# Optimization experiments

Hardware: AMD Instinct MI355X
Metric: run time of the kernel (lower is better)

Reference implementation:

```python
import jax, jax.numpy as jnp
import numpy as np

EPS = 1e-5  # torch LayerNorm default


def setup_inputs() -> dict:
    key = jax.random.key(0)
    k_x, k_wc, k_w = jax.random.split(key, 3)
    B, S, D = 16, 512, 2048
    x = jax.random.normal(k_x, (B, S, D), dtype=jnp.float32)
    # LayerNorm params
    gamma = jnp.ones((D,), dtype=jnp.float32)
    beta = jnp.zeros((D,), dtype=jnp.float32)
    # router (spatial_cls) Linear(d_ffn, 4)
    Wc = jax.random.normal(k_wc, (D, 4), dtype=jnp.float32) * 0.02
    bc = jnp.zeros((4,), dtype=jnp.float32)
    # 4 pointwise Conv1d experts: kernel size 1 over seq channels -> [4, S, S]
    W = jax.random.normal(k_w, (4, S, S), dtype=jnp.float32) * (1.0 / np.sqrt(S))
    # biases initialised to constants -1.0, -0.5, 0.5, 1.0 per expert
    b = jnp.stack([
        jnp.full((S,), -1.0, dtype=jnp.float32),
        jnp.full((S,), -0.5, dtype=jnp.float32),
        jnp.full((S,), 0.5, dtype=jnp.float32),
        jnp.full((S,), 1.0, dtype=jnp.float32),
    ])
    return {"x": x, "gamma": gamma, "beta": beta, "Wc": Wc, "bc": bc, "W": W, "b": b}


def reference(x, gamma, beta, Wc, bc, W, b):
    # LayerNorm over last dim
    mu = jnp.mean(x, axis=-1, keepdims=True)
    var = jnp.mean(jnp.square(x - mu), axis=-1, keepdims=True)
    y = (x - mu) * jax.lax.rsqrt(var + EPS) * gamma + beta
    # router: computed as in the original, but (faithfully to the source bug)
    # NOT used for dispatch -- dispatch uses the batch index n, clamped to 3.
    cls = jax.nn.softmax(y[:, 0] @ Wc + bc, axis=-1)
    _cls_idx = jnp.argmax(cls, axis=-1)  # computed, unused (original bug)
    eidx = jnp.minimum(jnp.arange(x.shape[0]), 3)  # sample n -> expert min(n,3)
    # pointwise Conv1d == seq-mixing matmul: out[b,s,d] = sum_t W_e[s,t] y[b,t,d] + b_e[s]
    out = jnp.einsum('bst,btd->bsd', W[eidx], y) + b[eidx][:, :, None]
    return jax.nn.gelu(out, approximate=False) + x
```

## Files before the change

### kernel.cpp

```cpp
#include <hip/hip_runtime.h>
#include <hip/hip_bf16.h>
#include <math.h>

#define NB 16
#define NS 512
#define ND 2048

typedef __attribute__((ext_vector_type(4))) float  f32x4v;
typedef __attribute__((ext_vector_type(8))) short  short8v;
typedef __attribute__((ext_vector_type(4))) float  accv;

__device__ __forceinline__ unsigned short f2bf(float f) {
  union { float f; unsigned u; } v; v.f = f;
  unsigned r = v.u + 0x7FFFu + ((v.u >> 16) & 1u);
  return (unsigned short)(r >> 16);
}

__device__ __forceinline__ int swz(int r, int kq) { return r * 4 + (kq ^ ((r >> 1) & 3)); }

#define GLL16(gp, lp) __builtin_amdgcn_global_load_lds(                        \
    (const __attribute__((address_space(1))) void*)(gp),                       \
    (__attribute__((address_space(3))) void*)(lp), 16, 0, 0)

__global__ __launch_bounds__(256) void k_meanvar(const float* __restrict__ x,
                                                 float* __restrict__ mv) {
  int row  = blockIdx.x * 4 + (threadIdx.x >> 6);
  int lane = threadIdx.x & 63;
  const float* xr = x + (size_t)row * ND;
  float s = 0.f, ss = 0.f;
#pragma unroll
  for (int q = 0; q < 8; ++q) {
    f32x4v v = *reinterpret_cast<const f32x4v*>(xr + q * 256 + lane * 4);
#pragma unroll
    for (int j = 0; j < 4; ++j) { s += v[j]; ss += v[j] * v[j]; }
  }
#pragma unroll
  for (int off = 1; off < 64; off <<= 1) {
    s  += __shfl_xor(s, off);
    ss += __shfl_xor(ss, off);
  }
  if (lane == 0) {
    float mean = s * (1.0f / ND);
    float var  = ss * (1.0f / ND) - mean * mean;
    mv[2 * row]     = mean;
    mv[2 * row + 1] = rsqrtf(var + 1e-5f);
  }
}

__global__ __launch_bounds__(256) void k_wcvt(const float* __restrict__ W,
                                              unsigned short* __restrict__ Aimg) {
  int ks = blockIdx.x, mp = blockIdx.y, e = blockIdx.z;
  size_t img = ((size_t)(e * 4 + mp) * 16 + ks) * 4096;
  int tid = threadIdx.x;
#pragma unroll
  for (int u = 0; u < 2; ++u) {
    int p = u * 256 + tid;
    int r = p >> 2, cc = p & 3;
    int kq = cc ^ ((r >> 1) & 3);
    const float* src = W + ((size_t)e * NS + mp * 128 + r) * NS + ks * 32 + kq * 8;
    f32x4v v0 = *reinterpret_cast<const f32x4v*>(src);
    f32x4v v1 = *reinterpret_cast<const f32x4v*>(src + 4);
    short8v o;
#pragma unroll
    for (int j = 0; j < 4; ++j) { o[j] = (short)f2bf(v0[j]); o[4 + j] = (short)f2bf(v1[j]); }
    *reinterpret_cast<short8v*>(Aimg + img + (size_t)p * 8) = o;
  }
}

__global__ __launch_bounds__(256) void k_normT(const float* __restrict__ x,
                                               const float* __restrict__ mv,
                                               const float* __restrict__ gamma,
                                               const float* __restrict__ beta,
                                               unsigned short* __restrict__ Bimg) {
  int d0 = blockIdx.x * 64, t0 = blockIdx.y * 64, bb = blockIdx.z;
  __shared__ unsigned int lds[64 * 32];
  int tid = threadIdx.x;
  {
    int tl = tid >> 2;
    int c  = tid & 3;
    int trow = bb * NS + t0 + tl;
    float mean = mv[2 * trow], rstd = mv[2 * trow + 1];
    const float* xr = x + (size_t)trow * ND + d0;
    int k = tl & 31;
#pragma unroll
    for (int q = 0; q < 4; ++q) {
      int dl = c * 16 + q * 4;
      f32x4v v = *reinterpret_cast<const f32x4v*>(xr + dl);
      f32x4v g = *reinterpret_cast<const f32x4v*>(gamma + d0 + dl);
      f32x4v b = *reinterpret_cast<const f32x4v*>(beta + d0 + dl);
      unsigned short h[4];
#pragma unroll
      for (int j = 0; j < 4; ++j) h[j] = f2bf((v[j] - mean) * rstd * g[j] + b[j]);
      lds[tl * 32 + (((dl >> 1)    ) ^ k)] = (unsigned)h[0] | ((unsigned)h[1] << 16);
      lds[tl * 32 + (((dl >> 1) + 1) ^ k)] = (unsigned)h[2] | ((unsigned)h[3] << 16);
    }
  }
  __syncthreads();
  {
    int dl = tid >> 2;
    int tc = (tid & 3) * 16;
    short8v o0, o1;
#pragma unroll
    for (int i = 0; i < 16; ++i) {
      int t = tc + i;
      unsigned w = lds[t * 32 + ((dl >> 1) ^ (t & 31))];
      unsigned short val = (dl & 1) ? (unsigned short)(w >> 16)
                                    : (unsigned short)(w & 0xffffu);
      if (i < 8) o0[i] = (short)val; else o1[i - 8] = (short)val;
    }
    int d  = d0 + dl;
    int np = d >> 7, r = d & 127;
    int tb  = t0 + tc;
    int ks  = tb >> 5;
    int kq0 = (tb >> 3) & 3;
    size_t img = ((size_t)(bb * 16 + np) * 16 + ks) * 4096;
    *reinterpret_cast<short8v*>(Bimg + img + (size_t)swz(r, kq0)     * 8) = o0;
    *reinterpret_cast<short8v*>(Bimg + img + (size_t)swz(r, kq0 + 1) * 8) = o1;
  }
}

__global__ __launch_bounds__(256) void k_gemm(const unsigned short* __restrict__ Aimg,
                                              const unsigned short* __restrict__ Bimg,
                                              const float* __restrict__ bias,
                                              const float* __restrict__ x,
                                              float* __restrict__ out) {
  int np = blockIdx.x, mp = blockIdx.y, bb = blockIdx.z;
  int e = bb < 3 ? bb : 3;
  const char* Abase = (const char*)(Aimg + ((size_t)(e  * 4 + mp) * 16) * 4096);
  const char* Bbase = (const char*)(Bimg + ((size_t)(bb * 16 + np) * 16) * 4096);
  __shared__ unsigned short Al[4096];
  __shared__ unsigned short Bl[4096];
  int tid = threadIdx.x;
  int lane = tid & 63, wid = tid >> 6;
  int wr = wid >> 1, wc = wid & 1;
  int lr = lane & 15, kq = lane >> 4;

  int aoff[4], boff[4];
#pragma unroll
  for (int mi = 0; mi < 4; ++mi) { int rr = wr * 64 + mi * 16 + lr; aoff[mi] = swz(rr, kq) * 8; }
#pragma unroll
  for (int ni = 0; ni < 4; ++ni) { int rr = wc * 64 + ni * 16 + lr; boff[ni] = swz(rr, kq) * 8; }

  accv acc[4][4] = {};

  for (int ks = 0; ks < 16; ++ks) {
#pragma unroll
    for (int i = 0; i < 2; ++i) {
      GLL16(Abase + ks * 8192 + i * 4096 + tid * 16, (char*)Al + i * 4096 + wid * 1024);
      GLL16(Bbase + ks * 8192 + i * 4096 + tid * 16, (char*)Bl + i * 4096 + wid * 1024);
    }
    __syncthreads();
    short8v a[4], b[4];
#pragma unroll
    for (int mi = 0; mi < 4; ++mi) a[mi] = *reinterpret_cast<const short8v*>(&Al[aoff[mi]]);
#pragma unroll
    for (int ni = 0; ni < 4; ++ni) b[ni] = *reinterpret_cast<const short8v*>(&Bl[boff[ni]]);
#pragma unroll
    for (int mi = 0; mi < 4; ++mi)
#pragma unroll
      for (int ni = 0; ni < 4; ++ni)
        acc[mi][ni] = __builtin_amdgcn_mfma_f32_16x16x32_bf16(a[mi], b[ni], acc[mi][ni], 0, 0, 0);
    __syncthreads();
  }

  const float* bp = bias + (size_t)e * NS;
  int m0 = mp * 128, n0 = np * 128;
#pragma unroll
  for (int mi = 0; mi < 4; ++mi) {
#pragma unroll
    for (int ni = 0; ni < 4; ++ni) {
#pragma unroll
      for (int r = 0; r < 4; ++r) {
        int s = m0 + wr * 64 + mi * 16 + ((lane >> 4) * 4) + r;
        int d = n0 + wc * 64 + ni * 16 + (lane & 15);
        float v = acc[mi][ni][r] + bp[s];
        float u = 1.5957691216f * (v + 0.044715f * v * v * v);
        float g = v / (1.0f + __expf(-u));
        size_t idx = ((size_t)bb * NS + s) * ND + d;
        out[idx] = g + x[idx];
      }
    }
  }
}

extern "C" void kernel_launch(void* const* d_in, const int* in_sizes, int n_in,
                              void* d_out, int out_size, void* d_ws, size_t ws_size,
                              hipStream_t stream) {
  const float* x     = (const float*)d_in[0];
  const float* gamma = (const float*)d_in[1];
  const float* beta  = (const float*)d_in[2];
  const float* W     = (const float*)d_in[5];
  const float* bias  = (const float*)d_in[6];
  float* out = (float*)d_out;

  unsigned short* Aimg = (unsigned short*)d_ws;
  float*          mv   = (float*)((char*)d_ws + (2ull << 20));
  unsigned short* Bimg = (unsigned short*)((char*)d_ws + (2ull << 20) + (64ull << 10));

  k_meanvar<<<NB * NS / 4, 256, 0, stream>>>(x, mv);
  k_wcvt<<<dim3(16, 4, 4), 256, 0, stream>>>(W, Aimg);
  k_normT<<<dim3(ND / 64, NS / 64, NB), 256, 0, stream>>>(x, mv, gamma, beta, Bimg);
  k_gemm<<<dim3(ND / 128, NS / 128, NB), 256, 0, stream>>>(Aimg, Bimg, bias, x, out);
}
```

Baseline: 177.0 us.

## Fuse LayerNorm stats into transpose kernel and double-buffer GEMM LDS loads

Merges the mean/variance pass and the normalize-transpose pass into one kernel that keeps each row in registers, so x is read once instead of twice. The normalized bf16 output is now written as a plain transposed [d][t] array. The GEMM swizzles that array on load through global_load_lds and double-buffers its LDS tiles, which removes one barrier per k-step. The cost is heavy register use in the LN kernel and more shared memory in the GEMM.

```diff
diff --git a/kernel.cpp b/kernel.cpp
--- a/kernel.cpp
+++ b/kernel.cpp
@@ -22,31 +22,6 @@
     (const __attribute__((address_space(1))) void*)(gp),                       \
     (__attribute__((address_space(3))) void*)(lp), 16, 0, 0)
 
-__global__ __launch_bounds__(256) void k_meanvar(const float* __restrict__ x,
-                                                 float* __restrict__ mv) {
-  int row  = blockIdx.x * 4 + (threadIdx.x >> 6);
-  int lane = threadIdx.x & 63;
-  const float* xr = x + (size_t)row * ND;
-  float s = 0.f, ss = 0.f;
-#pragma unroll
-  for (int q = 0; q < 8; ++q) {
-    f32x4v v = *reinterpret_cast<const f32x4v*>(xr + q * 256 + lane * 4);
-#pragma unroll
-    for (int j = 0; j < 4; ++j) { s += v[j]; ss += v[j] * v[j]; }
-  }
-#pragma unroll
-  for (int off = 1; off < 64; off <<= 1) {
-    s  += __shfl_xor(s, off);
-    ss += __shfl_xor(ss, off);
-  }
-  if (lane == 0) {
-    float mean = s * (1.0f / ND);
-    float var  = ss * (1.0f / ND) - mean * mean;
-    mv[2 * row]     = mean;
-    mv[2 * row + 1] = rsqrtf(var + 1e-5f);
-  }
-}
-
 __global__ __launch_bounds__(256) void k_wcvt(const float* __restrict__ W,
                                               unsigned short* __restrict__ Aimg) {
   int ks = blockIdx.x, mp = blockIdx.y, e = blockIdx.z;
@@ -67,69 +42,72 @@
   }
 }
 
-__global__ __launch_bounds__(256) void k_normT(const float* __restrict__ x,
-                                               const float* __restrict__ mv,
-                                               const float* __restrict__ gamma,
-                                               const float* __restrict__ beta,
-                                               unsigned short* __restrict__ Bimg) {
-  int d0 = blockIdx.x * 64, t0 = blockIdx.y * 64, bb = blockIdx.z;
-  __shared__ unsigned int lds[64 * 32];
+__global__ __launch_bounds__(512) void k_ln(const float* __restrict__ x,
+                                            const float* __restrict__ gamma,
+                                            const float* __restrict__ beta,
+                                            unsigned short* __restrict__ yT) {
+  int t0 = blockIdx.x * 32;
+  int bb = blockIdx.y;
   int tid = threadIdx.x;
-  {
-    int tl = tid >> 2;
-    int c  = tid & 3;
-    int trow = bb * NS + t0 + tl;
-    float mean = mv[2 * trow], rstd = mv[2 * trow + 1];
-    const float* xr = x + (size_t)trow * ND + d0;
-    int k = tl & 31;
+  int tA  = tid >> 4;
+  int dqA = (tid & 15) * 4;
+  const float* xr = x + ((size_t)bb * NS + t0 + tA) * ND + dqA;
+  f32x4v xv[32];
 #pragma unroll
-    for (int q = 0; q < 4; ++q) {
-      int dl = c * 16 + q * 4;
-      f32x4v v = *reinterpret_cast<const f32x4v*>(xr + dl);
-      f32x4v g = *reinterpret_cast<const f32x4v*>(gamma + d0 + dl);
-      f32x4v b = *reinterpret_cast<const f32x4v*>(beta + d0 + dl);
-      unsigned short h[4];
+  for (int k = 0; k < 32; ++k) xv[k] = *reinterpret_cast<const f32x4v*>(xr + k * 64);
+  float s = 0.f, ss = 0.f;
 #pragma unroll
-      for (int j = 0; j < 4; ++j) h[j] = f2bf((v[j] - mean) * rstd * g[j] + b[j]);
-      lds[tl * 32 + (((dl >> 1)    ) ^ k)] = (unsigned)h[0] | ((unsigned)h[1] << 16);
-      lds[tl * 32 + (((dl >> 1) + 1) ^ k)] = (unsigned)h[2] | ((unsigned)h[3] << 16);
+  for (int k = 0; k < 32; ++k)
+#pragma unroll
+    for (int j = 0; j < 4; ++j) { float f = xv[k][j]; s += f; ss += f * f; }
+#pragma unroll
+  for (int off = 1; off < 16; off <<= 1) {
+    s  += __shfl_xor(s, off);
+    ss += __shfl_xor(ss, off);
+  }
+  float mean = s * (1.0f / ND);
+  float rstd = rsqrtf(ss * (1.0f / ND) - mean * mean + 1e-5f);
+
+  __shared__ unsigned tw[2][1024];
+  int dlR = tid >> 3;
+  int tcR = (tid & 7) * 4;
+  unsigned short* yTb = yT + (size_t)bb * ND * NS + t0;
+  int wb = dqA >> 1;
+#pragma unroll
+  for (int k = 0; k < 32; ++k) {
+    int d0 = k * 64;
+    f32x4v g = *reinterpret_cast<const f32x4v*>(gamma + d0 + dqA);
+    f32x4v b = *reinterpret_cast<const f32x4v*>(beta  + d0 + dqA);
+    unsigned short h[4];
+#pragma unroll
+    for (int j = 0; j < 4; ++j) h[j] = f2bf((xv[k][j] - mean) * rstd * g[j] + b[j]);
+    unsigned* twb = tw[k & 1];
+    twb[tA * 32 + ((wb    ) ^ tA)] = (unsigned)h[0] | ((unsigned)h[1] << 16);
+    twb[tA * 32 + ((wb + 1) ^ tA)] = (unsigned)h[2] | ((unsigned)h[3] << 16);
+    __syncthreads();
+    unsigned short o[4];
+#pragma unroll
+    for (int i = 0; i < 4; ++i) {
+      int t = tcR + i;
+      unsigned w = twb[t * 32 + ((dlR >> 1) ^ t)];
+      o[i] = (dlR & 1) ? (unsigned short)(w >> 16) : (unsigned short)(w & 0xffffu);
     }
-  }
-  __syncthreads();
-  {
-    int dl = tid >> 2;
-    int tc = (tid & 3) * 16;
-    short8v o0, o1;
-#pragma unroll
-    for (int i = 0; i < 16; ++i) {
-      int t = tc + i;
-      unsigned w = lds[t * 32 + ((dl >> 1) ^ (t & 31))];
-      unsigned short val = (dl & 1) ? (unsigned short)(w >> 16)
-                                    : (unsigned short)(w & 0xffffu);
-      if (i < 8) o0[i] = (short)val; else o1[i - 8] = (short)val;
-    }
-    int d  = d0 + dl;
-    int np = d >> 7, r = d & 127;
-    int tb  = t0 + tc;
-    int ks  = tb >> 5;
-    int kq0 = (tb >> 3) & 3;
-    size_t img = ((size_t)(bb * 16 + np) * 16 + ks) * 4096;
-    *reinterpret_cast<short8v*>(Bimg + img + (size_t)swz(r, kq0)     * 8) = o0;
-    *reinterpret_cast<short8v*>(Bimg + img + (size_t)swz(r, kq0 + 1) * 8) = o1;
+    *reinterpret_cast<ushort4*>(yTb + (size_t)(d0 + dlR) * NS + tcR) =
+        make_ushort4(o[0], o[1], o[2], o[3]);
   }
 }
 
 __global__ __launch_bounds__(256) void k_gemm(const unsigned short* __restrict__ Aimg,
-                                              const unsigned short* __restrict__ Bimg,
+                                              const unsigned short* __restrict__ yT,
                                               const float* __restrict__ bias,
                                               const float* __restrict__ x,
                                               float* __restrict__ out) {
   int np = blockIdx.x, mp = blockIdx.y, bb = blockIdx.z;
   int e = bb < 3 ? bb : 3;
-  const char* Abase = (const char*)(Aimg + ((size_t)(e  * 4 + mp) * 16) * 4096);
-  const char* Bbase = (const char*)(Bimg + ((size_t)(bb * 16 + np) * 16) * 4096);
-  __shared__ unsigned short Al[4096];
-  __shared__ unsigned short Bl[4096];
+  const char* Abase = (const char*)(Aimg + ((size_t)(e * 4 + mp) * 16) * 4096);
+  int n0 = np * 128;
+  __shared__ unsigned short Al[2][4096];
+  __shared__ unsigned short Bl[2][4096];
   int tid = threadIdx.x;
   int lane = tid & 63, wid = tid >> 6;
   int wr = wid >> 1, wc = wid & 1;
@@ -141,30 +119,41 @@
 #pragma unroll
   for (int ni = 0; ni < 4; ++ni) { int rr = wc * 64 + ni * 16 + lr; boff[ni] = swz(rr, kq) * 8; }
 
+  int rs = tid >> 2, cs = tid & 3;
+  int kqs = cs ^ ((rs >> 1) & 3);
+  const char* Bsrc = (const char*)(yT + (size_t)bb * ND * NS + (size_t)(n0 + rs) * NS) + kqs * 16;
+
   accv acc[4][4] = {};
 
+#define STAGE(bufi, ks)                                                                  \
+  do {                                                                                   \
+    GLL16(Abase + (ks) * 8192 +        tid * 16, (char*)Al[bufi] +        wid * 1024);   \
+    GLL16(Abase + (ks) * 8192 + 4096 + tid * 16, (char*)Al[bufi] + 4096 + wid * 1024);   \
+    GLL16(Bsrc  + (ks) * 64,                     (char*)Bl[bufi] +        wid * 1024);   \
+    GLL16(Bsrc  + (ks) * 64 + 65536,             (char*)Bl[bufi] + 4096 + wid * 1024);   \
+  } while (0)
+
+  STAGE(0, 0);
   for (int ks = 0; ks < 16; ++ks) {
-#pragma unroll
-    for (int i = 0; i < 2; ++i) {
-      GLL16(Abase + ks * 8192 + i * 4096 + tid * 16, (char*)Al + i * 4096 + wid * 1024);
-      GLL16(Bbase + ks * 8192 + i * 4096 + tid * 16, (char*)Bl + i * 4096 + wid * 1024);
-    }
     __syncthreads();
+    if (ks < 15) STAGE((ks + 1) & 1, ks + 1);
+    const unsigned short* Ab = Al[ks & 1];
+    const unsigned short* Bb = Bl[ks & 1];
     short8v a[4], b[4];
 #pragma unroll
-    for (int mi = 0; mi < 4; ++mi) a[mi] = *reinterpret_cast<const short8v*>(&Al[aoff[mi]]);
+    for (int mi = 0; mi < 4; ++mi) a[mi] = *reinterpret_cast<const short8v*>(&Ab[aoff[mi]]);
 #pragma unroll
-    for (int ni = 0; ni < 4; ++ni) b[ni] = *reinterpret_cast<const short8v*>(&Bl[boff[ni]]);
+    for (int ni = 0; ni < 4; ++ni) b[ni] = *reinterpret_cast<const short8v*>(&Bb[boff[ni]]);
 #pragma unroll
     for (int mi = 0; mi < 4; ++mi)
 #pragma unroll
       for (int ni = 0; ni < 4; ++ni)
         acc[mi][ni] = __builtin_amdgcn_mfma_f32_16x16x32_bf16(a[mi], b[ni], acc[mi][ni], 0, 0, 0);
-    __syncthreads();
   }
+#undef STAGE
 
   const float* bp = bias + (size_t)e * NS;
-  int m0 = mp * 128, n0 = np * 128;
+  int m0 = mp * 128;
 #pragma unroll
   for (int mi = 0; mi < 4; ++mi) {
 #pragma unroll
@@ -194,11 +183,9 @@
   float* out = (float*)d_out;
 
   unsigned short* Aimg = (unsigned short*)d_ws;
-  float*          mv   = (float*)((char*)d_ws + (2ull << 20));
-  unsigned short* Bimg = (unsigned short*)((char*)d_ws + (2ull << 20) + (64ull << 10));
+  unsigned short* yT   = (unsigned short*)((char*)d_ws + (2ull << 20));
 
-  k_meanvar<<<NB * NS / 4, 256, 0, stream>>>(x, mv);
   k_wcvt<<<dim3(16, 4, 4), 256, 0, stream>>>(W, Aimg);
-  k_normT<<<dim3(ND / 64, NS / 64, NB), 256, 0, stream>>>(x, mv, gamma, beta, Bimg);
-  k_gemm<<<dim3(ND / 128, NS / 128, NB), 256, 0, stream>>>(Aimg, Bimg, bias, x, out);
+  k_ln<<<dim3(NS / 32, NB), 512, 0, stream>>>(x, gamma, beta, yT);
+  k_gemm<<<dim3(ND / 128, NS / 128, NB), 256, 0, stream>>>(Aimg, yT, bias, x, out);
 }
```

Result: slower. 198.4 us (+12.1%).

## Triple-buffer GEMM LDS loads and shrink LayerNorm-transpose tile

Applied to the files above, without the earlier changes.

The GEMM main loop now keeps three LDS buffers and issues async global-to-LDS loads two K-steps ahead. It waits with explicit vmcnt counters and a single barrier per step instead of two __syncthreads. This is meant to hide global load latency behind MFMA work, at the cost of three times the LDS footprint, which may lower occupancy. The LayerNorm-transpose kernel now uses 32-row tiles with one 16-byte store per thread, and the workspace layout is rearranged so the stats buffer sits after Bimg.

```diff
diff --git a/kernel.cpp b/kernel.cpp
--- a/kernel.cpp
+++ b/kernel.cpp
@@ -22,8 +22,8 @@
     (const __attribute__((address_space(1))) void*)(gp),                       \
     (__attribute__((address_space(3))) void*)(lp), 16, 0, 0)
 
-__global__ __launch_bounds__(256) void k_meanvar(const float* __restrict__ x,
-                                                 float* __restrict__ mv) {
+__global__ __launch_bounds__(256) void k_stats(const float* __restrict__ x,
+                                               float* __restrict__ mv) {
   int row  = blockIdx.x * 4 + (threadIdx.x >> 6);
   int lane = threadIdx.x & 63;
   const float* xr = x + (size_t)row * ND;
@@ -67,55 +67,54 @@
   }
 }
 
-__global__ __launch_bounds__(256) void k_normT(const float* __restrict__ x,
-                                               const float* __restrict__ mv,
-                                               const float* __restrict__ gamma,
-                                               const float* __restrict__ beta,
-                                               unsigned short* __restrict__ Bimg) {
-  int d0 = blockIdx.x * 64, t0 = blockIdx.y * 64, bb = blockIdx.z;
-  __shared__ unsigned int lds[64 * 32];
+__global__ __launch_bounds__(256) void k_lnT(const float* __restrict__ x,
+                                             const float* __restrict__ mv,
+                                             const float* __restrict__ gamma,
+                                             const float* __restrict__ beta,
+                                             unsigned short* __restrict__ Bimg) {
+  int d0 = blockIdx.x * 64, t0 = blockIdx.y * 32, bb = blockIdx.z;
+  __shared__ unsigned tw[1024];
   int tid = threadIdx.x;
   {
-    int tl = tid >> 2;
-    int c  = tid & 3;
-    int trow = bb * NS + t0 + tl;
-    float mean = mv[2 * trow], rstd = mv[2 * trow + 1];
-    const float* xr = x + (size_t)trow * ND + d0;
-    int k = tl & 31;
-#pragma unroll
-    for (int q = 0; q < 4; ++q) {
-      int dl = c * 16 + q * 4;
-      f32x4v v = *reinterpret_cast<const f32x4v*>(xr + dl);
-      f32x4v g = *reinterpret_cast<const f32x4v*>(gamma + d0 + dl);
-      f32x4v b = *reinterpret_cast<const f32x4v*>(beta + d0 + dl);
-      unsigned short h[4];
-#pragma unroll
-      for (int j = 0; j < 4; ++j) h[j] = f2bf((v[j] - mean) * rstd * g[j] + b[j]);
-      lds[tl * 32 + (((dl >> 1)    ) ^ k)] = (unsigned)h[0] | ((unsigned)h[1] << 16);
-      lds[tl * 32 + (((dl >> 1) + 1) ^ k)] = (unsigned)h[2] | ((unsigned)h[3] << 16);
+    int tA = tid >> 3;
+    int dq = (tid & 7) * 8;
+    int row = bb * NS + t0 + tA;
+    float mean = mv[2 * row], rstd = mv[2 * row + 1];
+    const float* xr = x + (size_t)row * ND + d0 + dq;
+    f32x4v v0 = *reinterpret_cast<const f32x4v*>(xr);
+    f32x4v v1 = *reinterpret_cast<const f32x4v*>(xr + 4);
+    f32x4v g0 = *reinterpret_cast<const f32x4v*>(gamma + d0 + dq);
+    f32x4v g1 = *reinterpret_cast<const f32x4v*>(gamma + d0 + dq + 4);
+    f32x4v b0 = *reinterpret_cast<const f32x4v*>(beta + d0 + dq);
+    f32x4v b1 = *reinterpret_cast<const f32x4v*>(beta + d0 + dq + 4);
+    unsigned short h[8];
+#pragma unroll
+    for (int j = 0; j < 4; ++j) {
+      h[j]     = f2bf((v0[j] - mean) * rstd * g0[j] + b0[j]);
+      h[4 + j] = f2bf((v1[j] - mean) * rstd * g1[j] + b1[j]);
     }
+    int wb = dq >> 1;
+#pragma unroll
+    for (int q = 0; q < 4; ++q)
+      tw[tA * 32 + ((wb + q) ^ tA)] = (unsigned)h[2 * q] | ((unsigned)h[2 * q + 1] << 16);
   }
   __syncthreads();
   {
     int dl = tid >> 2;
-    int tc = (tid & 3) * 16;
-    short8v o0, o1;
-#pragma unroll
-    for (int i = 0; i < 16; ++i) {
-      int t = tc + i;
-      unsigned w = lds[t * 32 + ((dl >> 1) ^ (t & 31))];
-      unsigned short val = (dl & 1) ? (unsigned short)(w >> 16)
-                                    : (unsigned short)(w & 0xffffu);
-      if (i < 8) o0[i] = (short)val; else o1[i - 8] = (short)val;
+    int th = (tid & 3) * 8;
+    short8v o;
+#pragma unroll
+    for (int i = 0; i < 8; ++i) {
+      int t = th + i;
+      unsigned w = tw[t * 32 + ((dl >> 1) ^ t)];
+      o[i] = (short)((dl & 1) ? (unsigned short)(w >> 16) : (unsigned short)(w & 0xffffu));
     }
     int d  = d0 + dl;
-    int np = d >> 7, r = d & 127;
-    int tb  = t0 + tc;
-    int ks  = tb >> 5;
-    int kq0 = (tb >> 3) & 3;
+    int r  = d & 127, np = d >> 7;
+    int ks = t0 >> 5;
+    int kq = th >> 3;
     size_t img = ((size_t)(bb * 16 + np) * 16 + ks) * 4096;
-    *reinterpret_cast<short8v*>(Bimg + img + (size_t)swz(r, kq0)     * 8) = o0;
-    *reinterpret_cast<short8v*>(Bimg + img + (size_t)swz(r, kq0 + 1) * 8) = o1;
+    *reinterpret_cast<short8v*>(Bimg + img + (size_t)swz(r, kq) * 8) = o;
   }
 }
 
@@ -128,8 +127,8 @@
   int e = bb < 3 ? bb : 3;
   const char* Abase = (const char*)(Aimg + ((size_t)(e  * 4 + mp) * 16) * 4096);
   const char* Bbase = (const char*)(Bimg + ((size_t)(bb * 16 + np) * 16) * 4096);
-  __shared__ unsigned short Al[4096];
-  __shared__ unsigned short Bl[4096];
+  __shared__ unsigned short Al[3 * 4096];
+  __shared__ unsigned short Bl[3 * 4096];
   int tid = threadIdx.x;
   int lane = tid & 63, wid = tid >> 6;
   int wr = wid >> 1, wc = wid & 1;
@@ -143,25 +142,38 @@
 
   accv acc[4][4] = {};
 
+#define STAGE(p, ks)                                                                     \
+  do {                                                                                   \
+    GLL16(Abase + (ks) * 8192 +        tid * 16, (char*)Al + (p) * 8192 +        wid * 1024); \
+    GLL16(Abase + (ks) * 8192 + 4096 + tid * 16, (char*)Al + (p) * 8192 + 4096 + wid * 1024); \
+    GLL16(Bbase + (ks) * 8192 +        tid * 16, (char*)Bl + (p) * 8192 +        wid * 1024); \
+    GLL16(Bbase + (ks) * 8192 + 4096 + tid * 16, (char*)Bl + (p) * 8192 + 4096 + wid * 1024); \
+  } while (0)
+
+  STAGE(0, 0);
+  STAGE(1, 1);
+#pragma unroll
   for (int ks = 0; ks < 16; ++ks) {
-#pragma unroll
-    for (int i = 0; i < 2; ++i) {
-      GLL16(Abase + ks * 8192 + i * 4096 + tid * 16, (char*)Al + i * 4096 + wid * 1024);
-      GLL16(Bbase + ks * 8192 + i * 4096 + tid * 16, (char*)Bl + i * 4096 + wid * 1024);
-    }
-    __syncthreads();
+    if (ks == 15) asm volatile("s_waitcnt vmcnt(0)" ::: "memory");
+    else          asm volatile("s_waitcnt vmcnt(4)" ::: "memory");
+    __builtin_amdgcn_s_barrier();
+    __builtin_amdgcn_sched_barrier(0);
+    if (ks + 2 < 16) STAGE((ks + 2) % 3, ks + 2);
+    const unsigned short* Ab = Al + (ks % 3) * 4096;
+    const unsigned short* Bb = Bl + (ks % 3) * 4096;
     short8v a[4], b[4];
 #pragma unroll
-    for (int mi = 0; mi < 4; ++mi) a[mi] = *reinterpret_cast<const short8v*>(&Al[aoff[mi]]);
-#pragma unroll
-    for (int ni = 0; ni < 4; ++ni) b[ni] = *reinterpret_cast<const short8v*>(&Bl[boff[ni]]);
+    for (int mi = 0; mi < 4; ++mi) a[mi] = *reinterpret_cast<const short8v*>(&Ab[aoff[mi]]);
+#pragma unroll
+    for (int ni = 0; ni < 4; ++ni) b[ni] = *reinterpret_cast<const short8v*>(&Bb[boff[ni]]);
 #pragma unroll
     for (int mi = 0; mi < 4; ++mi)
 #pragma unroll
       for (int ni = 0; ni < 4; ++ni)
         acc[mi][ni] = __builtin_amdgcn_mfma_f32_16x16x32_bf16(a[mi], b[ni], acc[mi][ni], 0, 0, 0);
-    __syncthreads();
-  }
+    asm volatile("" ::: "memory");
+  }
+#undef STAGE
 
   const float* bp = bias + (size_t)e * NS;
   int m0 = mp * 128, n0 = np * 128;
@@ -172,7 +184,7 @@
 #pragma unroll
       for (int r = 0; r < 4; ++r) {
         int s = m0 + wr * 64 + mi * 16 + ((lane >> 4) * 4) + r;
-        int d = n0 + wc * 64 + ni * 16 + (lane & 15);
+        int d = n0 + wc * 64 + ni * 16 + lr;
         float v = acc[mi][ni][r] + bp[s];
         float u = 1.5957691216f * (v + 0.044715f * v * v * v);
         float g = v / (1.0f + __expf(-u));
@@ -194,11 +206,11 @@
   float* out = (float*)d_out;
 
   unsigned short* Aimg = (unsigned short*)d_ws;
-  float*          mv   = (float*)((char*)d_ws + (2ull << 20));
-  unsigned short* Bimg = (unsigned short*)((char*)d_ws + (2ull << 20) + (64ull << 10));
-
-  k_meanvar<<<NB * NS / 4, 256, 0, stream>>>(x, mv);
+  unsigned short* Bimg = (unsigned short*)((char*)d_ws + (2ull << 20));
+  float*          mv   = (float*)((char*)d_ws + (34ull << 20));
+
+  k_stats<<<NB * NS / 4, 256, 0, stream>>>(x, mv);
   k_wcvt<<<dim3(16, 4, 4), 256, 0, stream>>>(W, Aimg);
-  k_normT<<<dim3(ND / 64, NS / 64, NB), 256, 0, stream>>>(x, mv, gamma, beta, Bimg);
+  k_lnT<<<dim3(ND / 64, NS / 32, NB), 256, 0, stream>>>(x, mv, gamma, beta, Bimg);
   k_gemm<<<dim3(ND / 128, NS / 128, NB), 256, 0, stream>>>(Aimg, Bimg, bias, x, out);
 }
```

Result: no change. 175.6 us (-0.8%).
